# Kernel optimization log

Hardware: AMD Instinct MI355X
Metric: run time of the kernel (lower is better)

Reference implementation:

```python
import jax, jax.numpy as jnp
import numpy as np

GAMMA, LMBD, EPS = 0.99, 0.95, 0.2
T, D, H, A = 262144, 128, 256, 8


def _mlp_gauss(x, W1, b1, Wmu, bmu, Wlv, blv):
    h = jnp.tanh(x @ W1 + b1)
    return h @ Wmu + bmu, h @ Wlv + blv  # mu, logvar: [T, A]


def _critic(x, Wc1, bc1, Wc2, bc2):
    h = jnp.tanh(x @ Wc1 + bc1)
    return h @ Wc2 + bc2  # [T, 1]


def setup_inputs() -> dict:
    key = jax.random.key(0)
    ks = jax.random.split(key, 12)
    s = 0.05  # small init scale for stable exp()/ratio
    return {
        "state": jax.random.normal(ks[0], (T, D), jnp.float32),
        "next_state": jax.random.normal(ks[1], (T, D), jnp.float32),
        "action": jax.random.normal(ks[2], (T, A), jnp.float32),
        "beta_log_prob": jax.random.normal(ks[3], (T, A), jnp.float32) * 0.1,
        "reward": jax.random.normal(ks[4], (T,), jnp.float32),
        "W1": jax.random.normal(ks[5], (D, H), jnp.float32) * s,
        "b1": jnp.zeros((H,), jnp.float32),
        "Wmu": jax.random.normal(ks[6], (H, A), jnp.float32) * s,
        "bmu": jnp.zeros((A,), jnp.float32),
        "Wlv": jax.random.normal(ks[7], (H, A), jnp.float32) * s,
        "blv": jnp.zeros((A,), jnp.float32),
        "Wc1": jax.random.normal(ks[8], (D, H), jnp.float32) * s,
        "bc1": jnp.zeros((H,), jnp.float32),
        "Wc2": jax.random.normal(ks[9], (H, 1), jnp.float32) * s,
        "bc2": jnp.zeros((1,), jnp.float32),
    }


def reference(state, next_state, action, beta_log_prob, reward,
              W1, b1, Wmu, bmu, Wlv, blv, Wc1, bc1, Wc2, bc2):
    # critic values
    value = _critic(state, Wc1, bc1, Wc2, bc2)            # [T, 1]
    v0 = value[:, 0]                                       # [T]
    v1 = _critic(next_state, Wc1, bc1, Wc2, bc2)[:, 0]     # [T]

    # GAE: reverse recurrence gae_t = delta_t + gamma*lambda*gae_{t+1}
    delta = reward + GAMMA * v1 - v0                       # [T]

    def step(g, d):
        g = d + GAMMA * LMBD * g
        return g, g

    _, gae_rev = jax.lax.scan(step, jnp.float32(0.0), delta[::-1])
    # torch code rebuilds each gae into a fresh Tensor -> returns are detached
    ret = jax.lax.stop_gradient(gae_rev[::-1][:, None])    # [T, 1]

    advantage = ret - value                                # [T, 1] (grad via value)
    a_hat = (advantage - advantage.mean()) / (jnp.std(advantage, ddof=1) + 1e-7)

    # pi log-prob of actions under Normal(mu, sqrt(exp(logvar)))
    mu, logvar = _mlp_gauss(state, W1, b1, Wmu, bmu, Wlv, blv)  # [T, A]
    log_2pi = jnp.float32(np.log(2.0 * np.pi))
    pi_lp = -0.5 * ((action - mu) ** 2) * jnp.exp(-logvar) - 0.5 * logvar - 0.5 * log_2pi

    ratio = jnp.exp(jnp.sum(pi_lp - jax.lax.stop_gradient(beta_log_prob),
                            axis=1, keepdims=True))        # [T, 1]

    actor_loss = -jnp.sum(jnp.minimum(ratio * a_hat,
                                      jnp.clip(ratio, 1.0 - EPS, 1.0 + EPS) * a_hat))
    critic_loss = jnp.sum(advantage ** 2)
    return actor_loss + critic_loss
```

## Files before the change

kernel.cpp:

```cpp
#include <hip/hip_runtime.h>

#define T_N   262144
#define D_IN  128
#define H_HID 256
#define A_DIM 8
#define GAMMA 0.99f
#define EPS_C 0.2f
#define C_GL  0.9405f
#define HALF_LOG_2PI 0.9189385332f
#define SCALE2 2.8853900817779268f
#define ST_TPB 16
#define NX_TPB 8

typedef __attribute__((ext_vector_type(8))) short short8;
typedef __attribute__((ext_vector_type(4))) float f32x4;

__device__ __forceinline__ unsigned short f2bf(float f) {
  unsigned int u = __float_as_uint(f);
  u += 0x7FFFu + ((u >> 16) & 1u);
  return (unsigned short)(u >> 16);
}
__device__ __forceinline__ float tanh_pre(float a) {
  float e = __builtin_amdgcn_exp2f(a);
  return 1.f - 2.f * __builtin_amdgcn_rcpf(e + 1.f);
}
__device__ __forceinline__ float row16_sum(float p) {
  p += __int_as_float(__builtin_amdgcn_update_dpp(0, __float_as_int(p), 0x111, 0xf, 0xf, true));
  p += __int_as_float(__builtin_amdgcn_update_dpp(0, __float_as_int(p), 0x112, 0xf, 0xf, true));
  p += __int_as_float(__builtin_amdgcn_update_dpp(0, __float_as_int(p), 0x114, 0xf, 0xf, true));
  p += __int_as_float(__builtin_amdgcn_update_dpp(0, __float_as_int(p), 0x118, 0xf, 0xf, true));
  return p;
}

__global__ __launch_bounds__(256) void k_prep(
    const float* __restrict__ Wc1, const float* __restrict__ W1,
    const float* __restrict__ Wmu, const float* __restrict__ Wlv,
    unsigned short* __restrict__ Wc1Ts, unsigned short* __restrict__ W1Ts,
    unsigned short* __restrict__ H1) {
  int i = blockIdx.x * 256 + threadIdx.x;
  if (i < 32768) {
    int n = i >> 7, k = i & 127;
    Wc1Ts[i] = f2bf(Wc1[k * 256 + n] * SCALE2);
  } else if (i < 65536) {
    int j = i - 32768; int n = j >> 7, k = j & 127;
    W1Ts[j] = f2bf(W1[k * 256 + n] * SCALE2);
  } else if (i < 69632) {
    int j = i - 65536; int h = j >> 8, n = j & 255;
    H1[j] = (h < 8) ? f2bf(Wmu[n * 8 + h]) : f2bf(Wlv[n * 8 + (h - 8)]);
  }
}

__global__ __launch_bounds__(512, 4) void k_state(
    const float* __restrict__ state,
    const float* __restrict__ action, const float* __restrict__ beta_lp,
    const unsigned short* __restrict__ Wc1Ts, const unsigned short* __restrict__ W1Ts,
    const unsigned short* __restrict__ H1,
    const float* __restrict__ bc1, const float* __restrict__ b1,
    const float* __restrict__ Wc2, const float* __restrict__ bc2,
    const float* __restrict__ bmu, const float* __restrict__ blv,
    float* __restrict__ v0out, float* __restrict__ ratio) {
  const int tid  = threadIdx.x;
  const int lane = tid & 63;
  const int wv   = tid >> 6;
  const int role = wv >> 2;
  const int wl   = wv & 3;
  const int c    = lane & 15;
  const int quad = lane >> 4;

  __shared__ unsigned short sh_x[32 * 136];
  __shared__ unsigned short sh_h[32 * 264];
  __shared__ float sh_hb[4 * 32 * 16];
  __shared__ float sh_v[32 * 4];

  const unsigned short* WT = role ? W1Ts : Wc1Ts;
  const float* bias = role ? b1 : bc1;

  short8 bfrag[4][4];
  float bias_c[4], wc2_c[4];
#pragma unroll
  for (int ct = 0; ct < 4; ++ct) {
    int n = wl * 64 + ct * 16 + c;
    bias_c[ct] = bias[n] * SCALE2;
    wc2_c[ct]  = Wc2[n];
#pragma unroll
    for (int ki = 0; ki < 4; ++ki)
      bfrag[ct][ki] = *(const short8*)(WT + n * 128 + ki * 32 + quad * 8);
  }
  const float vbias = bc2[0];
  const int aa = tid & 7;
  const float bmu_a = bmu[aa], blv_a = blv[aa];

  const int t0 = blockIdx.x * ST_TPB;

  float4 rbuf[2];
  {
    const float4* Xv = (const float4*)(state + t0 * 32 * D_IN);
    rbuf[0] = Xv[tid]; rbuf[1] = Xv[tid + 512];
  }

  for (int i = 0; i < ST_TPB; ++i) {
    const int r0 = (t0 + i) * 32;

#pragma unroll
    for (int j = 0; j < 2; ++j) {
      int e4 = tid + j * 512;
      int row = e4 >> 5, c4 = e4 & 31;
      ushort4 u;
      u.x = f2bf(rbuf[j].x); u.y = f2bf(rbuf[j].y);
      u.z = f2bf(rbuf[j].z); u.w = f2bf(rbuf[j].w);
      *(ushort4*)(&sh_x[row * 136 + c4 * 4]) = u;
    }
    __syncthreads();

    if (i + 1 < ST_TPB) {
      const float4* Xv2 = (const float4*)(state + (r0 + 32) * D_IN);
      rbuf[0] = Xv2[tid]; rbuf[1] = Xv2[tid + 512];
    }
    float fa = 0.f, fb = 0.f;
    if (tid < 256) { fa = action[r0 * 8 + tid]; fb = beta_lp[r0 * 8 + tid]; }

    if (role == 0) {
#pragma unroll
      for (int rt = 0; rt < 2; ++rt) {
        f32x4 acc[4];
#pragma unroll
        for (int ct = 0; ct < 4; ++ct) acc[ct] = (f32x4){0.f, 0.f, 0.f, 0.f};
#pragma unroll
        for (int ki = 0; ki < 4; ++ki) {
          short8 a = *(const short8*)(&sh_x[(rt * 16 + c) * 136 + ki * 32 + quad * 8]);
#pragma unroll
          for (int ct = 0; ct < 4; ++ct)
            acc[ct] = __builtin_amdgcn_mfma_f32_16x16x32_bf16(a, bfrag[ct][ki], acc[ct], 0, 0, 0);
        }
#pragma unroll
        for (int r = 0; r < 4; ++r) {
          float p = 0.f;
#pragma unroll
          for (int ct = 0; ct < 4; ++ct)
            p += tanh_pre(acc[ct][r] + bias_c[ct]) * wc2_c[ct];
          p = row16_sum(p);
          if (c == 15) sh_v[(rt * 16 + quad * 4 + r) * 4 + wl] = p;
        }
      }
    } else {
#pragma unroll
      for (int rt = 0; rt < 2; ++rt) {
        f32x4 acc[4];
#pragma unroll
        for (int ct = 0; ct < 4; ++ct) acc[ct] = (f32x4){0.f, 0.f, 0.f, 0.f};
#pragma unroll
        for (int ki = 0; ki < 4; ++ki) {
          short8 a = *(const short8*)(&sh_x[(rt * 16 + c) * 136 + ki * 32 + quad * 8]);
#pragma unroll
          for (int ct = 0; ct < 4; ++ct)
            acc[ct] = __builtin_amdgcn_mfma_f32_16x16x32_bf16(a, bfrag[ct][ki], acc[ct], 0, 0, 0);
        }
#pragma unroll
        for (int ct = 0; ct < 4; ++ct) {
          int col = wl * 64 + ct * 16 + c;
#pragma unroll
          for (int r = 0; r < 4; ++r) {
            int row = rt * 16 + quad * 4 + r;
            sh_h[row * 264 + col] = f2bf(tanh_pre(acc[ct][r] + bias_c[ct]));
          }
        }
      }
    }
    __syncthreads();

    if (role == 1) {
#pragma unroll
      for (int st = 0; st < 2; ++st) {
        f32x4 acc2 = (f32x4){0.f, 0.f, 0.f, 0.f};
#pragma unroll
        for (int k2 = 0; k2 < 2; ++k2) {
          int kofs = wl * 64 + k2 * 32 + quad * 8;
          short8 a2 = *(const short8*)(H1 + c * 256 + kofs);
          short8 b2 = *(const short8*)(&sh_h[(st * 16 + c) * 264 + kofs]);
          acc2 = __builtin_amdgcn_mfma_f32_16x16x32_bf16(a2, b2, acc2, 0, 0, 0);
        }
        *((f32x4*)&sh_hb[((wl * 32) + st * 16 + c) * 16 + quad * 4]) = acc2;
      }
    } else if (tid < 32) {
      v0out[r0 + tid] = sh_v[tid * 4] + sh_v[tid * 4 + 1] + sh_v[tid * 4 + 2] +
                        sh_v[tid * 4 + 3] + vbias;
    }
    __syncthreads();

    if (tid < 256) {
      int s = tid >> 3;
      float mu = sh_hb[(s)*16 + aa]          + sh_hb[(32 + s) * 16 + aa] +
                 sh_hb[(64 + s) * 16 + aa]   + sh_hb[(96 + s) * 16 + aa] + bmu_a;
      float lv = sh_hb[(s)*16 + 8 + aa]      + sh_hb[(32 + s) * 16 + 8 + aa] +
                 sh_hb[(64 + s) * 16 + 8 + aa] + sh_hb[(96 + s) * 16 + 8 + aa] + blv_a;
      float d = fa - mu;
      float term = -0.5f * d * d * __expf(-lv) - 0.5f * lv - HALF_LOG_2PI - fb;
      term += __shfl_xor(term, 1);
      term += __shfl_xor(term, 2);
      term += __shfl_xor(term, 4);
      if (aa == 0) ratio[r0 + s] = __expf(term);
    }
  }
}

__global__ __launch_bounds__(256, 4) void k_next(
    const float* __restrict__ next_state,
    const unsigned short* __restrict__ Wc1Ts,
    const float* __restrict__ bc1, const float* __restrict__ Wc2,
    const float* __restrict__ bc2, float* __restrict__ v1out) {
  const int tid = threadIdx.x;
  const int lane = tid & 63;
  const int wv   = tid >> 6;
  const int c    = lane & 15;
  const int quad = lane >> 4;

  __shared__ unsigned short sh_x[32 * 136];
  __shared__ float sh_v[32 * 4];

  short8 bfrag[4][4];
  float bias_c[4], wc2_c[4];
#pragma unroll
  for (int ct = 0; ct < 4; ++ct) {
    int n = wv * 64 + ct * 16 + c;
    bias_c[ct] = bc1[n] * SCALE2;
    wc2_c[ct]  = Wc2[n];
#pragma unroll
    for (int ki = 0; ki < 4; ++ki)
      bfrag[ct][ki] = *(const short8*)(Wc1Ts + n * 128 + ki * 32 + quad * 8);
  }
  const float vbias = bc2[0];

  const int t0 = blockIdx.x * NX_TPB;
  float4 rbuf[4];
  {
    const float4* Xv = (const float4*)(next_state + t0 * 32 * D_IN);
#pragma unroll
    for (int j = 0; j < 4; ++j) rbuf[j] = Xv[tid + j * 256];
  }

  for (int i = 0; i < NX_TPB; ++i) {
    const int r0 = (t0 + i) * 32;
#pragma unroll
    for (int j = 0; j < 4; ++j) {
      int e = tid + j * 256;
      int row = e >> 5, c4 = e & 31;
      ushort4 u;
      u.x = f2bf(rbuf[j].x); u.y = f2bf(rbuf[j].y);
      u.z = f2bf(rbuf[j].z); u.w = f2bf(rbuf[j].w);
      *(ushort4*)(&sh_x[row * 136 + c4 * 4]) = u;
    }
    __syncthreads();

    if (i + 1 < NX_TPB) {
      const float4* Xv2 = (const float4*)(next_state + (r0 + 32) * D_IN);
#pragma unroll
      for (int j = 0; j < 4; ++j) rbuf[j] = Xv2[tid + j * 256];
    }

#pragma unroll
    for (int rt = 0; rt < 2; ++rt) {
      f32x4 acc[4];
#pragma unroll
      for (int ct = 0; ct < 4; ++ct) acc[ct] = (f32x4){0.f, 0.f, 0.f, 0.f};
#pragma unroll
      for (int ki = 0; ki < 4; ++ki) {
        short8 a = *(const short8*)(&sh_x[(rt * 16 + c) * 136 + ki * 32 + quad * 8]);
#pragma unroll
        for (int ct = 0; ct < 4; ++ct)
          acc[ct] = __builtin_amdgcn_mfma_f32_16x16x32_bf16(a, bfrag[ct][ki], acc[ct], 0, 0, 0);
      }
#pragma unroll
      for (int r = 0; r < 4; ++r) {
        float p = 0.f;
#pragma unroll
        for (int ct = 0; ct < 4; ++ct)
          p += tanh_pre(acc[ct][r] + bias_c[ct]) * wc2_c[ct];
        p = row16_sum(p);
        if (c == 15) sh_v[(rt * 16 + quad * 4 + r) * 4 + wv] = p;
      }
    }
    __syncthreads();
    if (tid < 32) {
      v1out[r0 + tid] = sh_v[tid * 4] + sh_v[tid * 4 + 1] + sh_v[tid * 4 + 2] +
                        sh_v[tid * 4 + 3] + vbias;
    }
  }
}

__global__ __launch_bounds__(256) void k_gae(
    const float* __restrict__ reward, const float* __restrict__ v0,
    const float* __restrict__ v1, float* __restrict__ adv,
    float* __restrict__ accs) {
  const int j = blockIdx.x, k = threadIdx.x;
  const int base = j * 1024 + k * 8;
  float d[8];
  float s = 0.f, w = 1.f;
#pragma unroll
  for (int i = 0; i < 8; ++i) {
    int idx = base + i;
    float dd = 0.f;
    if (idx < T_N) dd = reward[idx] + GAMMA * v1[idx] - v0[idx];
    d[i] = dd;
    s += w * dd;
    w *= C_GL;
  }
  const float W8 = w;
  __shared__ float Ss[256], Sw[256];
  Ss[k] = s; Sw[k] = W8;
  __syncthreads();
  for (int dd = 1; dd < 256; dd <<= 1) {
    bool has = (k + dd) < 256;
    float ns = 0.f, nw = 0.f;
    if (has) { ns = Ss[k] + Sw[k] * Ss[k + dd]; nw = Sw[k] * Sw[k + dd]; }
    __syncthreads();
    if (has) { Ss[k] = ns; Sw[k] = nw; }
    __syncthreads();
  }
  float g = (k < 255) ? Ss[k + 1] : 0.f;
  float sa = 0.f, sq = 0.f;
  if (k < 128) {
#pragma unroll
    for (int i = 7; i >= 0; --i) {
      g = d[i] + C_GL * g;
      float a = g - v0[base + i];
      adv[base + i] = a;
      sa += a; sq += a * a;
    }
  }
  __syncthreads();
  Ss[k] = sa; Sw[k] = sq;
  __syncthreads();
  for (int off = 128; off > 0; off >>= 1) {
    if (k < off) { Ss[k] += Ss[k + off]; Sw[k] += Sw[k + off]; }
    __syncthreads();
  }
  if (k == 0) {
    atomicAdd(&accs[0], Ss[0]);
    atomicAdd(&accs[1], Sw[0]);
  }
}

__global__ __launch_bounds__(256) void k_loss(
    const float* __restrict__ adv, const float* __restrict__ ratio,
    float* __restrict__ accs, float* __restrict__ out) {
  int t = blockIdx.x * 256 + threadIdx.x;
  float sum  = accs[0];
  float mean = sum * (1.f / (float)T_N);
  float var  = (accs[1] - sum * mean) / (float)(T_N - 1);
  float inv  = 1.f / (sqrtf(var) + 1e-7f);
  float a = (adv[t] - mean) * inv;
  float r = ratio[t];
  float rc = fminf(fmaxf(r, 1.f - EPS_C), 1.f + EPS_C);
  float term = -fminf(r * a, rc * a);
  __shared__ float red[256];
  int k = threadIdx.x;
  red[k] = term;
  __syncthreads();
  for (int off = 128; off > 0; off >>= 1) {
    if (k < off) red[k] += red[k + off];
    __syncthreads();
  }
  if (k == 0) {
    atomicAdd(&accs[2], red[0]);
    __threadfence();
    unsigned int old = atomicAdd((unsigned int*)&accs[3], 1u);
    if (old == (unsigned int)(gridDim.x - 1)) {
      __threadfence();
      volatile float* va = (volatile float*)accs;
      out[0] = va[2] + va[1];
    }
  }
}

extern "C" void kernel_launch(void* const* d_in, const int* in_sizes, int n_in,
                              void* d_out, int out_size, void* d_ws, size_t ws_size,
                              hipStream_t stream) {
  const float* state      = (const float*)d_in[0];
  const float* next_state = (const float*)d_in[1];
  const float* action     = (const float*)d_in[2];
  const float* beta_lp    = (const float*)d_in[3];
  const float* reward     = (const float*)d_in[4];
  const float* W1   = (const float*)d_in[5];
  const float* b1   = (const float*)d_in[6];
  const float* Wmu  = (const float*)d_in[7];
  const float* bmu  = (const float*)d_in[8];
  const float* Wlv  = (const float*)d_in[9];
  const float* blv  = (const float*)d_in[10];
  const float* Wc1  = (const float*)d_in[11];
  const float* bc1  = (const float*)d_in[12];
  const float* Wc2  = (const float*)d_in[13];
  const float* bc2  = (const float*)d_in[14];

  char* ws = (char*)d_ws;
  size_t o = 0;
  unsigned short* Wc1Ts = (unsigned short*)(ws + o); o += 65536;
  unsigned short* W1Ts  = (unsigned short*)(ws + o); o += 65536;
  unsigned short* H1    = (unsigned short*)(ws + o); o += 8192;
  float* v0    = (float*)(ws + o); o += (size_t)T_N * 4;
  float* v1    = (float*)(ws + o); o += (size_t)T_N * 4;
  float* ratio = (float*)(ws + o); o += (size_t)T_N * 4;
  float* adv   = (float*)(ws + o); o += (size_t)T_N * 4;
  float* accs  = (float*)(ws + o); o += 256;

  hipMemsetAsync(accs, 0, 32, stream);

  k_prep<<<272, 256, 0, stream>>>(Wc1, W1, Wmu, Wlv, Wc1Ts, W1Ts, H1);

  k_state<<<(T_N / 32) / ST_TPB, 512, 0, stream>>>(
      state, action, beta_lp, Wc1Ts, W1Ts, H1, bc1, b1, Wc2, bc2, bmu, blv,
      v0, ratio);
  k_next<<<(T_N / 32) / NX_TPB, 256, 0, stream>>>(
      next_state, Wc1Ts, bc1, Wc2, bc2, v1);
  k_gae<<<256, 256, 0, stream>>>(reward, v0, v1, adv, accs);
  k_loss<<<T_N / 256, 256, 0, stream>>>(adv, ratio, accs, (float*)d_out);
}
```

Before: 383.1 us.

## Fuse GAE and loss kernels via grid barrier, drop memset, retune tiles

Merges the GAE scan and the clipped-loss reduction into one kernel. Blocks wait at a spin barrier on a global counter for the advantage mean and variance, so advantages stay in registers and are never written to or read back from global memory. The accumulator memset moves into the prep kernel, saving a launch. It also halves rows per block in the state and next-state kernels for more blocks, packs bf16 conversion with perm, truncates hidden activations to bf16, pads the shared reduction buffer against bank conflicts, and uses DPP for the 8-lane sum. The spin barrier assumes all 256 blocks are co-resident, and truncation changes rounding slightly.

Result: faster. 375.4 us (-2.0%).

```diff
diff --git a/kernel.cpp b/kernel.cpp
--- a/kernel.cpp
+++ b/kernel.cpp
@@ -2,15 +2,15 @@
 
 #define T_N   262144
 #define D_IN  128
-#define H_HID 256
 #define A_DIM 8
 #define GAMMA 0.99f
 #define EPS_C 0.2f
 #define C_GL  0.9405f
 #define HALF_LOG_2PI 0.9189385332f
 #define SCALE2 2.8853900817779268f
-#define ST_TPB 16
-#define NX_TPB 8
+#define ST_TPB 8
+#define NX_TPB 4
+#define HB_S   20
 
 typedef __attribute__((ext_vector_type(8))) short short8;
 typedef __attribute__((ext_vector_type(4))) float f32x4;
@@ -20,15 +20,28 @@
   u += 0x7FFFu + ((u >> 16) & 1u);
   return (unsigned short)(u >> 16);
 }
+__device__ __forceinline__ unsigned int pack_bf2(float lo, float hi) {
+  return __builtin_amdgcn_perm(__float_as_uint(hi), __float_as_uint(lo), 0x07060302u);
+}
+__device__ __forceinline__ unsigned short bf_trunc(float f) {
+  return (unsigned short)(__float_as_uint(f) >> 16);
+}
 __device__ __forceinline__ float tanh_pre(float a) {
   float e = __builtin_amdgcn_exp2f(a);
   return 1.f - 2.f * __builtin_amdgcn_rcpf(e + 1.f);
 }
+template <int CTRL>
+__device__ __forceinline__ float dpp_add(float p) {
+  return p + __int_as_float(__builtin_amdgcn_update_dpp(
+                 0, __float_as_int(p), CTRL, 0xF, 0xF, true));
+}
 __device__ __forceinline__ float row16_sum(float p) {
-  p += __int_as_float(__builtin_amdgcn_update_dpp(0, __float_as_int(p), 0x111, 0xf, 0xf, true));
-  p += __int_as_float(__builtin_amdgcn_update_dpp(0, __float_as_int(p), 0x112, 0xf, 0xf, true));
-  p += __int_as_float(__builtin_amdgcn_update_dpp(0, __float_as_int(p), 0x114, 0xf, 0xf, true));
-  p += __int_as_float(__builtin_amdgcn_update_dpp(0, __float_as_int(p), 0x118, 0xf, 0xf, true));
+  p = dpp_add<0x111>(p); p = dpp_add<0x112>(p);
+  p = dpp_add<0x114>(p); p = dpp_add<0x118>(p);
+  return p;
+}
+__device__ __forceinline__ float xor8_sum(float p) {
+  p = dpp_add<0xB1>(p); p = dpp_add<0x4E>(p); p = dpp_add<0x141>(p);
   return p;
 }
 
@@ -36,8 +49,9 @@
     const float* __restrict__ Wc1, const float* __restrict__ W1,
     const float* __restrict__ Wmu, const float* __restrict__ Wlv,
     unsigned short* __restrict__ Wc1Ts, unsigned short* __restrict__ W1Ts,
-    unsigned short* __restrict__ H1) {
+    unsigned short* __restrict__ H1, float* __restrict__ accs) {
   int i = blockIdx.x * 256 + threadIdx.x;
+  if (blockIdx.x == 0 && threadIdx.x < 8) ((unsigned int*)accs)[threadIdx.x] = 0u;
   if (i < 32768) {
     int n = i >> 7, k = i & 127;
     Wc1Ts[i] = f2bf(Wc1[k * 256 + n] * SCALE2);
@@ -69,7 +83,7 @@
 
   __shared__ unsigned short sh_x[32 * 136];
   __shared__ unsigned short sh_h[32 * 264];
-  __shared__ float sh_hb[4 * 32 * 16];
+  __shared__ float sh_hb[4 * 32 * HB_S];
   __shared__ float sh_v[32 * 4];
 
   const unsigned short* WT = role ? W1Ts : Wc1Ts;
@@ -94,7 +108,7 @@
 
   float4 rbuf[2];
   {
-    const float4* Xv = (const float4*)(state + t0 * 32 * D_IN);
+    const float4* Xv = (const float4*)(state + (size_t)t0 * 32 * D_IN);
     rbuf[0] = Xv[tid]; rbuf[1] = Xv[tid + 512];
   }
 
@@ -105,15 +119,15 @@
     for (int j = 0; j < 2; ++j) {
       int e4 = tid + j * 512;
       int row = e4 >> 5, c4 = e4 & 31;
-      ushort4 u;
-      u.x = f2bf(rbuf[j].x); u.y = f2bf(rbuf[j].y);
-      u.z = f2bf(rbuf[j].z); u.w = f2bf(rbuf[j].w);
-      *(ushort4*)(&sh_x[row * 136 + c4 * 4]) = u;
+      uint2 u;
+      u.x = pack_bf2(rbuf[j].x, rbuf[j].y);
+      u.y = pack_bf2(rbuf[j].z, rbuf[j].w);
+      *(uint2*)(&sh_x[row * 136 + c4 * 4]) = u;
     }
     __syncthreads();
 
     if (i + 1 < ST_TPB) {
-      const float4* Xv2 = (const float4*)(state + (r0 + 32) * D_IN);
+      const float4* Xv2 = (const float4*)(state + (size_t)(r0 + 32) * D_IN);
       rbuf[0] = Xv2[tid]; rbuf[1] = Xv2[tid + 512];
     }
     float fa = 0.f, fb = 0.f;
@@ -161,7 +175,7 @@
 #pragma unroll
           for (int r = 0; r < 4; ++r) {
             int row = rt * 16 + quad * 4 + r;
-            sh_h[row * 264 + col] = f2bf(tanh_pre(acc[ct][r] + bias_c[ct]));
+            sh_h[row * 264 + col] = bf_trunc(tanh_pre(acc[ct][r] + bias_c[ct]));
           }
         }
       }
@@ -179,7 +193,7 @@
           short8 b2 = *(const short8*)(&sh_h[(st * 16 + c) * 264 + kofs]);
           acc2 = __builtin_amdgcn_mfma_f32_16x16x32_bf16(a2, b2, acc2, 0, 0, 0);
         }
-        *((f32x4*)&sh_hb[((wl * 32) + st * 16 + c) * 16 + quad * 4]) = acc2;
+        *((f32x4*)&sh_hb[((wl * 32) + st * 16 + c) * HB_S + quad * 4]) = acc2;
       }
     } else if (tid < 32) {
       v0out[r0 + tid] = sh_v[tid * 4] + sh_v[tid * 4 + 1] + sh_v[tid * 4 + 2] +
@@ -189,15 +203,13 @@
 
     if (tid < 256) {
       int s = tid >> 3;
-      float mu = sh_hb[(s)*16 + aa]          + sh_hb[(32 + s) * 16 + aa] +
-                 sh_hb[(64 + s) * 16 + aa]   + sh_hb[(96 + s) * 16 + aa] + bmu_a;
-      float lv = sh_hb[(s)*16 + 8 + aa]      + sh_hb[(32 + s) * 16 + 8 + aa] +
-                 sh_hb[(64 + s) * 16 + 8 + aa] + sh_hb[(96 + s) * 16 + 8 + aa] + blv_a;
+      float mu = sh_hb[(s)*HB_S + aa]            + sh_hb[(32 + s) * HB_S + aa] +
+                 sh_hb[(64 + s) * HB_S + aa]     + sh_hb[(96 + s) * HB_S + aa] + bmu_a;
+      float lv = sh_hb[(s)*HB_S + 8 + aa]        + sh_hb[(32 + s) * HB_S + 8 + aa] +
+                 sh_hb[(64 + s) * HB_S + 8 + aa] + sh_hb[(96 + s) * HB_S + 8 + aa] + blv_a;
       float d = fa - mu;
       float term = -0.5f * d * d * __expf(-lv) - 0.5f * lv - HALF_LOG_2PI - fb;
-      term += __shfl_xor(term, 1);
-      term += __shfl_xor(term, 2);
-      term += __shfl_xor(term, 4);
+      term = xor8_sum(term);
       if (aa == 0) ratio[r0 + s] = __expf(term);
     }
   }
@@ -233,7 +245,7 @@
   const int t0 = blockIdx.x * NX_TPB;
   float4 rbuf[4];
   {
-    const float4* Xv = (const float4*)(next_state + t0 * 32 * D_IN);
+    const float4* Xv = (const float4*)(next_state + (size_t)t0 * 32 * D_IN);
 #pragma unroll
     for (int j = 0; j < 4; ++j) rbuf[j] = Xv[tid + j * 256];
   }
@@ -244,15 +256,15 @@
     for (int j = 0; j < 4; ++j) {
       int e = tid + j * 256;
       int row = e >> 5, c4 = e & 31;
-      ushort4 u;
-      u.x = f2bf(rbuf[j].x); u.y = f2bf(rbuf[j].y);
-      u.z = f2bf(rbuf[j].z); u.w = f2bf(rbuf[j].w);
-      *(ushort4*)(&sh_x[row * 136 + c4 * 4]) = u;
+      uint2 u;
+      u.x = pack_bf2(rbuf[j].x, rbuf[j].y);
+      u.y = pack_bf2(rbuf[j].z, rbuf[j].w);
+      *(uint2*)(&sh_x[row * 136 + c4 * 4]) = u;
     }
     __syncthreads();
 
     if (i + 1 < NX_TPB) {
-      const float4* Xv2 = (const float4*)(next_state + (r0 + 32) * D_IN);
+      const float4* Xv2 = (const float4*)(next_state + (size_t)(r0 + 32) * D_IN);
 #pragma unroll
       for (int j = 0; j < 4; ++j) rbuf[j] = Xv2[tid + j * 256];
     }
@@ -287,12 +299,15 @@
   }
 }
 
-__global__ __launch_bounds__(256) void k_gae(
+__global__ __launch_bounds__(256) void k_gae2(
     const float* __restrict__ reward, const float* __restrict__ v0,
-    const float* __restrict__ v1, float* __restrict__ adv,
-    float* __restrict__ accs) {
+    const float* __restrict__ v1, const float* __restrict__ ratio,
+    float* __restrict__ accs, float* __restrict__ out) {
   const int j = blockIdx.x, k = threadIdx.x;
   const int base = j * 1024 + k * 8;
+  unsigned int* cnt1 = (unsigned int*)accs + 4;
+  unsigned int* cnt2 = (unsigned int*)accs + 5;
+
   float d[8];
   float s = 0.f, w = 1.f;
 #pragma unroll
@@ -306,24 +321,26 @@
   }
   const float W8 = w;
   __shared__ float Ss[256], Sw[256];
+  __shared__ float sh_stats[2];
   Ss[k] = s; Sw[k] = W8;
   __syncthreads();
-  for (int dd = 1; dd < 256; dd <<= 1) {
-    bool has = (k + dd) < 256;
+  for (int st = 1; st < 256; st <<= 1) {
+    bool has = (k + st) < 256;
     float ns = 0.f, nw = 0.f;
-    if (has) { ns = Ss[k] + Sw[k] * Ss[k + dd]; nw = Sw[k] * Sw[k + dd]; }
+    if (has) { ns = Ss[k] + Sw[k] * Ss[k + st]; nw = Sw[k] * Sw[k + st]; }
     __syncthreads();
     if (has) { Ss[k] = ns; Sw[k] = nw; }
     __syncthreads();
   }
   float g = (k < 255) ? Ss[k + 1] : 0.f;
+  float adv[8];
   float sa = 0.f, sq = 0.f;
   if (k < 128) {
 #pragma unroll
     for (int i = 7; i >= 0; --i) {
       g = d[i] + C_GL * g;
       float a = g - v0[base + i];
-      adv[base + i] = a;
+      adv[i] = a;
       sa += a; sq += a * a;
     }
   }
@@ -337,37 +354,43 @@
   if (k == 0) {
     atomicAdd(&accs[0], Ss[0]);
     atomicAdd(&accs[1], Sw[0]);
-  }
-}
-
-__global__ __launch_bounds__(256) void k_loss(
-    const float* __restrict__ adv, const float* __restrict__ ratio,
-    float* __restrict__ accs, float* __restrict__ out) {
-  int t = blockIdx.x * 256 + threadIdx.x;
-  float sum  = accs[0];
-  float mean = sum * (1.f / (float)T_N);
-  float var  = (accs[1] - sum * mean) / (float)(T_N - 1);
-  float inv  = 1.f / (sqrtf(var) + 1e-7f);
-  float a = (adv[t] - mean) * inv;
-  float r = ratio[t];
-  float rc = fminf(fmaxf(r, 1.f - EPS_C), 1.f + EPS_C);
-  float term = -fminf(r * a, rc * a);
-  __shared__ float red[256];
-  int k = threadIdx.x;
-  red[k] = term;
+    __hip_atomic_fetch_add(cnt1, 1u, __ATOMIC_RELEASE, __HIP_MEMORY_SCOPE_AGENT);
+    while (__hip_atomic_load(cnt1, __ATOMIC_ACQUIRE, __HIP_MEMORY_SCOPE_AGENT) < 256u)
+      __builtin_amdgcn_s_sleep(4);
+    sh_stats[0] = __hip_atomic_load(&accs[0], __ATOMIC_RELAXED, __HIP_MEMORY_SCOPE_AGENT);
+    sh_stats[1] = __hip_atomic_load(&accs[1], __ATOMIC_RELAXED, __HIP_MEMORY_SCOPE_AGENT);
+  }
+  __syncthreads();
+
+  const float sum  = sh_stats[0];
+  const float cl   = sh_stats[1];
+  const float mean = sum * (1.f / (float)T_N);
+  const float var  = (cl - sum * mean) / (float)(T_N - 1);
+  const float inv  = 1.f / (sqrtf(var) + 1e-7f);
+  float sl = 0.f;
+  if (k < 128) {
+#pragma unroll
+    for (int i = 0; i < 8; ++i) {
+      float a = (adv[i] - mean) * inv;
+      float r = ratio[base + i];
+      float rc = fminf(fmaxf(r, 1.f - EPS_C), 1.f + EPS_C);
+      sl += -fminf(r * a, rc * a);
+    }
+  }
+  __syncthreads();
+  Ss[k] = sl;
   __syncthreads();
   for (int off = 128; off > 0; off >>= 1) {
-    if (k < off) red[k] += red[k + off];
+    if (k < off) Ss[k] += Ss[k + off];
     __syncthreads();
   }
   if (k == 0) {
-    atomicAdd(&accs[2], red[0]);
-    __threadfence();
-    unsigned int old = atomicAdd((unsigned int*)&accs[3], 1u);
-    if (old == (unsigned int)(gridDim.x - 1)) {
-      __threadfence();
-      volatile float* va = (volatile float*)accs;
-      out[0] = va[2] + va[1];
+    atomicAdd(&accs[2], Ss[0]);
+    unsigned int old = __hip_atomic_fetch_add(cnt2, 1u, __ATOMIC_ACQ_REL,
+                                              __HIP_MEMORY_SCOPE_AGENT);
+    if (old == 255u) {
+      float al = __hip_atomic_load(&accs[2], __ATOMIC_RELAXED, __HIP_MEMORY_SCOPE_AGENT);
+      out[0] = al + cl;
     }
   }
 }
@@ -399,18 +422,14 @@
   float* v0    = (float*)(ws + o); o += (size_t)T_N * 4;
   float* v1    = (float*)(ws + o); o += (size_t)T_N * 4;
   float* ratio = (float*)(ws + o); o += (size_t)T_N * 4;
-  float* adv   = (float*)(ws + o); o += (size_t)T_N * 4;
   float* accs  = (float*)(ws + o); o += 256;
 
-  hipMemsetAsync(accs, 0, 32, stream);
-
-  k_prep<<<272, 256, 0, stream>>>(Wc1, W1, Wmu, Wlv, Wc1Ts, W1Ts, H1);
+  k_prep<<<272, 256, 0, stream>>>(Wc1, W1, Wmu, Wlv, Wc1Ts, W1Ts, H1, accs);
 
   k_state<<<(T_N / 32) / ST_TPB, 512, 0, stream>>>(
       state, action, beta_lp, Wc1Ts, W1Ts, H1, bc1, b1, Wc2, bc2, bmu, blv,
       v0, ratio);
   k_next<<<(T_N / 32) / NX_TPB, 256, 0, stream>>>(
       next_state, Wc1Ts, bc1, Wc2, bc2, v1);
-  k_gae<<<256, 256, 0, stream>>>(reward, v0, v1, adv, accs);
-  k_loss<<<T_N / 256, 256, 0, stream>>>(adv, ratio, accs, (float*)d_out);
-}
+  k_gae2<<<256, 256, 0, stream>>>(reward, v0, v1, ratio, accs, (float*)d_out);
+}
```
